# Kernel optimization log

Hardware: AMD Instinct MI355X
Metric: run time of the kernel (lower is better)

## Reference

```python
import jax, jax.numpy as jnp
import numpy as np

B, S, I = 32, 256, 256      # batch, seq_len, input_size
H, N, C, O = 512, 128, 64, 256  # lstm hidden, mem addresses, content bits, output
P = 4 * C + 12              # head params: read(k,beta,g,s3,gamma) + write(same + erase + add)
EPS = 1e-8


def setup_inputs() -> dict:
    key = jax.random.key(0)
    ks = jax.random.split(key, 8)
    sc = 0.05
    return {
        "inputs_BxSxI": jax.random.normal(ks[0], (B, S, I), jnp.float32),
        "W_ih": jax.random.normal(ks[1], (4 * H, I + C), jnp.float32) * sc,
        "W_hh": jax.random.normal(ks[2], (4 * H, H), jnp.float32) * sc,
        "b_lstm": jnp.zeros((4 * H,), jnp.float32),
        "W_head": jax.random.normal(ks[3], (P, H), jnp.float32) * sc,
        "b_head": jnp.zeros((P,), jnp.float32),
        "W_out": jax.random.normal(ks[4], (O, H + C), jnp.float32) * sc,
        "b_out": jnp.zeros((O,), jnp.float32),
    }


def _address(k, beta, g, s, gamma, w_prev, M):
    """NTM addressing: content (cosine sim * beta softmax) -> gate -> circular shift -> sharpen."""
    Mn = M / (jnp.linalg.norm(M, axis=-1, keepdims=True) + EPS)   # [B,N,C]
    kn = k / (jnp.linalg.norm(k, axis=-1, keepdims=True) + EPS)   # [B,C]
    wc = jax.nn.softmax(beta * jnp.einsum('bnc,bc->bn', Mn, kn), axis=-1)
    wg = g * wc + (1.0 - g) * w_prev                              # interpolation gate
    ws = (s[:, 0:1] * jnp.roll(wg, -1, axis=-1)                   # 3-tap circular conv shift
          + s[:, 1:2] * wg
          + s[:, 2:3] * jnp.roll(wg, 1, axis=-1))
    wp = (ws + EPS) ** gamma                                      # sharpening, gamma >= 1
    return wp / jnp.sum(wp, axis=-1, keepdims=True)


def _forward(x, W_ih, W_hh, b_lstm, W_head, b_head, W_out, b_out):
    Bv = x.shape[0]
    splits = np.cumsum([C, 1, 1, 3, 1, C, 1, 1, 3, 1, C]).tolist()

    def step(state, x_t):
        M, w_r, w_w, r, h, c = state
        # LSTM controller on [input, prev_read]
        gates = jnp.concatenate([x_t, r], -1) @ W_ih.T + h @ W_hh.T + b_lstm
        gi, gf, gg, go = jnp.split(gates, 4, axis=-1)
        c = jax.nn.sigmoid(gf) * c + jax.nn.sigmoid(gi) * jnp.tanh(gg)
        h = jax.nn.sigmoid(go) * jnp.tanh(c)
        # interface parameters
        p = h @ W_head.T + b_head
        (k_r, b_r, g_r, s_r, gm_r,
         k_w, b_w, g_w, s_w, gm_w, e_w, a_w) = jnp.split(p, splits, axis=-1)
        w_r = _address(k_r, jax.nn.softplus(b_r), jax.nn.sigmoid(g_r),
                       jax.nn.softmax(s_r, axis=-1), 1.0 + jax.nn.softplus(gm_r), w_r, M)
        w_w = _address(k_w, jax.nn.softplus(b_w), jax.nn.sigmoid(g_w),
                       jax.nn.softmax(s_w, axis=-1), 1.0 + jax.nn.softplus(gm_w), w_w, M)
        # write (erase then add), then read
        e = jax.nn.sigmoid(e_w)
        M = M * (1.0 - w_w[:, :, None] * e[:, None, :]) + w_w[:, :, None] * a_w[:, None, :]
        r = jnp.einsum('bn,bnc->bc', w_r, M)
        out = jnp.concatenate([h, r], -1) @ W_out.T + b_out
        return (M, w_r, w_w, r, h, c), out

    w0 = jnp.zeros((Bv, N), jnp.float32).at[:, 0].set(1.0)
    init = (jnp.full((Bv, N, C), 0.01, jnp.float32), w0, w0,
            jnp.zeros((Bv, C), jnp.float32),
            jnp.zeros((Bv, H), jnp.float32), jnp.zeros((Bv, H), jnp.float32))
    _, outs = jax.lax.scan(step, init, jnp.swapaxes(x, 0, 1))  # [S,B,O]
    return jnp.swapaxes(outs, 0, 1)                            # [B,S,O]


def reference(inputs_BxSxI, W_ih, W_hh, b_lstm, W_head, b_head, W_out, b_out):
    return _forward(inputs_BxSxI, W_ih, W_hh, b_lstm, W_head, b_head, W_out, b_out)
```

## Files before the change

### kernel.cpp

```cpp
#include <hip/hip_runtime.h>
#include <hip/hip_fp16.h>
#include <math.h>

#define B_  32
#define S_  256
#define I_  256
#define H_  512
#define N_  128
#define C_  64
#define O_  256
#define P_  268
#define K_  832
#define HB  (H_*B_)
#define EPSX 1e-8f
#define NBLK 160
#define NPB  32
#define NGATE 128

#define OFF_XT   0
#define SZ_XT    (S_*I_*B_)
#define OFF_HA   (OFF_XT + SZ_XT)
#define SZ_HA    ((S_+1)*H_*B_)
#define OFF_RA   (OFF_HA + SZ_HA)
#define SZ_RA    ((S_+1)*C_*B_)
#define OFF_CT   (OFF_RA + SZ_RA)
#define SZ_CT    (H_*B_)
#define OFF_M    (OFF_CT + SZ_CT)
#define SZ_M     (B_*N_*C_)
#define OFF_WR   (OFF_M + SZ_M)
#define SZ_W     (B_*N_)
#define OFF_WW   (OFF_WR + SZ_W)
#define OFF_BAR  (OFF_WW + SZ_W)
#define SZ_BAR   8192
#define OFF_WOT  (OFF_BAR + SZ_BAR)
#define SZ_WOT   ((H_+C_)*O_)
#define OFF_WHH  (OFF_WOT + SZ_WOT)
#define SZ_WHH   ((P_*H_)/2)

__device__ __forceinline__ float sigm(float x) { return 1.f / (1.f + expf(-x)); }
__device__ __forceinline__ float splus(float x) {
    return fmaxf(x, 0.f) + log1pf(expf(-fabsf(x)));
}
__device__ __forceinline__ float wave_max(float v) {
    #pragma unroll
    for (int s = 1; s < 64; s <<= 1) v = fmaxf(v, __shfl_xor(v, s, 64));
    return v;
}
__device__ __forceinline__ float wave_sum(float v) {
    #pragma unroll
    for (int s = 1; s < 64; s <<= 1) v += __shfl_xor(v, s, 64);
    return v;
}

__device__ __forceinline__ void junk16(float& s) {
    #pragma unroll
    for (int d = 0; d < 16; ++d) s = fmaf(s, 1.0000001f, 1e-9f);
    asm volatile("" : "+v"(s));
}

__device__ __forceinline__ void wait_flags(unsigned* flags, int nf, unsigned tgt,
                                           volatile unsigned* ldsp, int tid)
{
    const int wv = tid >> 6, ln = tid & 63;
    if (wv < 2) {
        int idx = wv * 64 + ln;
        if (idx >= nf) idx = nf - 1;
        unsigned* p = &flags[idx * 16];
        float s = 1.f;
        for (;;) {
            unsigned v = __hip_atomic_load(p, __ATOMIC_RELAXED,
                                           __HIP_MEMORY_SCOPE_AGENT);
            if (__all((int)(v >= tgt))) break;
            junk16(s);
        }
        if (ln == 0) ldsp[wv] = tgt;
    } else {
        float s = (float)(tid + 1);
        while (ldsp[0] < tgt || ldsp[1] < tgt) junk16(s);
    }
    __syncthreads();
}

__global__ __launch_bounds__(256)
void prep_kernel(const float* __restrict__ x, const float* __restrict__ Wout,
                 const float* __restrict__ Whead, float* __restrict__ ws)
{
    int g = blockIdx.x * 256 + threadIdx.x;
    if (g < SZ_XT) {
        int b = g & 31, k = (g >> 5) & 255, t = g >> 13;
        ws[OFF_XT + g] = x[b * (S_*I_) + t * I_ + k];
        return;
    }
    g -= SZ_XT;
    if (g < SZ_WOT) {
        int o = g & 255, k = g >> 8;
        ws[OFF_WOT + g] = Wout[o * (H_ + C_) + k];
        return;
    }
    g -= SZ_WOT;
    if (g < HB)      { ws[OFF_HA + g] = 0.f;   return; }
    g -= HB;
    if (g < C_*B_)   { ws[OFF_RA + g] = 0.f;   return; }
    g -= C_*B_;
    if (g < SZ_CT)   { ws[OFF_CT + g] = 0.f;   return; }
    g -= SZ_CT;
    if (g < SZ_M)    { ws[OFF_M  + g] = 0.01f; return; }
    g -= SZ_M;
    if (g < 2*SZ_W)  { ws[OFF_WR + g] = 0.f;   return; }
    g -= 2*SZ_W;
    if (g < SZ_BAR)  { ws[OFF_BAR + g] = 0.f;  return; }
    g -= SZ_BAR;
    if (g < P_ * H_) {
        ((__half*)(ws + OFF_WHH))[g] = __float2half(Whead[g]);
        return;
    }
}

#define GEMM_STEP(khat, ap) {                                             \
    const float4 a0 = *(const float4*)(ap);                               \
    const float4 a1 = *(const float4*)((ap) + 4);                         \
    const float2 w01 = *(const float2*)&Wt[(khat) * 18 + (rg << 2)];      \
    const float2 w23 = *(const float2*)&Wt[(khat) * 18 + (rg << 2) + 2];  \
    const float wv[4] = {w01.x, w01.y, w23.x, w23.y};                     \
    const float av[8] = {a0.x, a0.y, a0.z, a0.w, a1.x, a1.y, a1.z, a1.w}; \
    _Pragma("unroll")                                                     \
    for (int j = 0; j < 4; ++j)                                           \
        _Pragma("unroll")                                                 \
        for (int bb = 0; bb < 8; ++bb)                                    \
            acc[j][bb] += wv[j] * av[bb]; }

__global__ __launch_bounds__(512)
void ntm_loop(const float* __restrict__ Wih, const float* __restrict__ Whh,
              const float* __restrict__ bl,  const float* __restrict__ bhead,
              float* __restrict__ ws)
{
    float* xT  = ws + OFF_XT;
    float* hA  = ws + OFF_HA;
    float* rA  = ws + OFF_RA;
    float* Mem = ws + OFF_M;
    unsigned* bar = (unsigned*)(ws + OFF_BAR);
    unsigned* flag_h = bar;
    unsigned* flag_r = bar + 4096;
    const unsigned short* whH = (const unsigned short*)(ws + OFF_WHH);

    __shared__ float Wt[K_ * 18];
    __shared__ float p_lds[P_];
    __shared__ float wldsR[128];
    __shared__ float wldsW[128];
    __shared__ float h_lds[H_];
    __shared__ unsigned syncf[4];

    const int tid  = threadIdx.x;
    const int bi   = blockIdx.x;
    const bool isPB = (bi < NPB);
    const int gi   = bi - NPB;

    if (tid < 4) syncf[tid] = 0;

    if (!isPB) {
        for (int idx = tid; idx < K_ * 16; idx += 512) {
            int rl = idx & 15, k = idx >> 4;
            int row = (rl & 3) * H_ + gi * 4 + (rl >> 2);
            float v = (k < I_ + C_) ? Wih[row * (I_ + C_) + k]
                                    : Whh[row * H_ + (k - (I_ + C_))];
            Wt[k * 18 + rl] = v;
        }
    } else if (tid < N_) {
        wldsR[tid] = (tid == 0) ? 1.f : 0.f;
        wldsW[tid] = (tid == 0) ? 1.f : 0.f;
    }
    __syncthreads();

    const int pair = tid >> 5;
    const int ks   = tid & 31;
    const int rg   = pair >> 2;
    const int bg   = pair & 3;
    const int b0   = bg * 8;

    float acc[4][8];
    float cr[8] = {0,0,0,0,0,0,0,0};
    float bI = 0, bF = 0, bG = 0, bO = 0;
    if (!isPB && ks == 0) {
        const int unit = gi * 4 + rg;
        bI = bl[unit];        bF = bl[H_ + unit];
        bG = bl[2*H_ + unit]; bO = bl[3*H_ + unit];
    }

    if (!isPB) {
        #pragma unroll
        for (int j = 0; j < 4; ++j)
            #pragma unroll
            for (int bb = 0; bb < 8; ++bb) acc[j][bb] = 0.f;
        const float* xs = xT;
        const float* hs = hA;
        #pragma unroll
        for (int i = 0; i < 8; ++i) {
            const int k = ks + (i << 5);
            GEMM_STEP(k, xs + k * B_ + b0);
        }
        #pragma unroll
        for (int i = 0; i < 16; ++i) {
            const int k = ks + (i << 5);
            GEMM_STEP(320 + k, hs + k * B_ + b0);
        }

        for (int t = 0; t < S_; ++t) {
            wait_flags(flag_r, NPB, (unsigned)t, &syncf[0], tid);

            const float* rs = rA + (size_t)t * C_ * B_;
            #pragma unroll
            for (int i = 0; i < 2; ++i) {
                const int k = ks + (i << 5);
                GEMM_STEP(256 + k, rs + k * B_ + b0);
            }
            #pragma unroll
            for (int j = 0; j < 4; ++j)
                #pragma unroll
                for (int bb = 0; bb < 8; ++bb) {
                    float v = acc[j][bb];
                    v += __shfl_xor(v, 16, 64);
                    v += __shfl_xor(v, 8, 64);
                    v += __shfl_xor(v, 4, 64);
                    v += __shfl_xor(v, 2, 64);
                    v += __shfl_xor(v, 1, 64);
                    acc[j][bb] = v;
                }
            if (ks == 0) {
                const int unit = gi * 4 + rg;
                #pragma unroll
                for (int bb = 0; bb < 8; ++bb) {
                    const int b = b0 + bb;
                    float gI = acc[0][bb] + bI;
                    float gF = acc[1][bb] + bF;
                    float gG = acc[2][bb] + bG;
                    float gO = acc[3][bb] + bO;
                    float cN = sigm(gF) * cr[bb] + sigm(gI) * tanhf(gG);
                    float hN = sigm(gO) * tanhf(cN);
                    cr[bb] = cN;
                    __hip_atomic_store(&hA[(size_t)(t + 1) * HB + unit * B_ + b],
                                       hN, __ATOMIC_RELAXED,
                                       __HIP_MEMORY_SCOPE_AGENT);
                }
            }
            __syncthreads();
            if (tid == 0) {
                asm volatile("s_waitcnt vmcnt(0) lgkmcnt(0)" ::: "memory");
                __hip_atomic_store(&flag_h[gi * 16], (unsigned)(t + 1),
                                   __ATOMIC_RELAXED, __HIP_MEMORY_SCOPE_AGENT);
            }
            wait_flags(flag_h, NGATE, (unsigned)(t + 1), &syncf[2], tid);

            #pragma unroll
            for (int j = 0; j < 4; ++j)
                #pragma unroll
                for (int bb = 0; bb < 8; ++bb) acc[j][bb] = 0.f;
            if (t + 1 < S_) {
                const float* xs2 = xT + (size_t)(t + 1) * I_ * B_;
                const float* hs2 = hA + (size_t)(t + 1) * HB;
                #pragma unroll
                for (int i = 0; i < 8; ++i) {
                    const int k = ks + (i << 5);
                    GEMM_STEP(k, xs2 + k * B_ + b0);
                }
                #pragma unroll
                for (int i = 0; i < 16; ++i) {
                    const int k = ks + (i << 5);
                    GEMM_STEP(320 + k, hs2 + k * B_ + b0);
                }
            }
        }
        return;
    }

    const int b = bi;
    float* Mb = Mem + (size_t)b * N_ * C_;
    for (int t = 0; t < S_; ++t) {
        wait_flags(flag_h, NGATE, (unsigned)(t + 1), &syncf[0], tid);

        const float* hs = hA + (size_t)(t + 1) * HB;
        h_lds[tid] = __hip_atomic_load(&hs[tid * B_ + b], __ATOMIC_RELAXED,
                                       __HIP_MEMORY_SCOPE_AGENT);
        __syncthreads();

        {
            const int sub  = tid & 1;
            const int row0 = tid >> 1;
            const float* hb = &h_lds[sub * 256];
            #pragma unroll
            for (int rep = 0; rep < 2; ++rep) {
                const int row = (rep == 0) ? row0
                              : ((row0 < P_ - 256) ? row0 + 256 : -1);
                if (row >= 0) {
                    const unsigned short* wrow = whH + row * H_ + sub * 256;
                    float acch = 0.f;
                    #pragma unroll 4
                    for (int k2 = 0; k2 < 256; k2 += 8) {
                        float4 raw = *(const float4*)&wrow[k2];
                        const __half2* hp = (const __half2*)&raw;
                        float2 f0 = __half22float2(hp[0]);
                        float2 f1 = __half22float2(hp[1]);
                        float2 f2 = __half22float2(hp[2]);
                        float2 f3 = __half22float2(hp[3]);
                        acch += f0.x * hb[k2]     + f0.y * hb[k2 + 1]
                              + f1.x * hb[k2 + 2] + f1.y * hb[k2 + 3]
                              + f2.x * hb[k2 + 4] + f2.y * hb[k2 + 5]
                              + f3.x * hb[k2 + 6] + f3.y * hb[k2 + 7];
                    }
                    acch += __shfl_xor(acch, 1, 64);
                    if (sub == 0) p_lds[row] = acch + bhead[row];
                }
            }
        }
        __syncthreads();

        {
            float* wtmpA = h_lds;
            float* sbufA = h_lds + 256;
            const int grp = (tid >> 7) & 1;
            const int l   = tid & 127;
            const bool act256 = (tid < 256);
            const int o = grp ? 70 : 0;
            const int widx = (tid >> 6) & 1;

            float z = 0.f, gate = 0.f, s0 = 0.f, s1 = 0.f, s2 = 0.f,
                  gamma = 1.f;
            if (act256) {
                float beta = splus(p_lds[o + 64]);
                gate = sigm(p_lds[o + 65]);
                float sa = p_lds[o + 66], sbv = p_lds[o + 67],
                      sc = p_lds[o + 68];
                float sm3 = fmaxf(sa, fmaxf(sbv, sc));
                float ea = __expf(sa - sm3), eb = __expf(sbv - sm3),
                      ec = __expf(sc - sm3);
                float es3 = ea + eb + ec;
                s0 = ea / es3; s1 = eb / es3; s2 = ec / es3;
                gamma = 1.f + splus(p_lds[o + 69]);
                float kk = 0.f;
                #pragma unroll 8
                for (int c = 0; c < C_; ++c) {
                    float kv = p_lds[o + c]; kk += kv * kv;
                }
                const float knorm = sqrtf(kk) + EPSX;
                float dot = 0.f, mm = 0.f;
                #pragma unroll
                for (int c = 0; c < C_; c += 4) {
                    float4 m4 = *(const float4*)&Mb[l * C_ + c];
                    dot += m4.x * p_lds[o + c]     + m4.y * p_lds[o + c + 1]
                         + m4.z * p_lds[o + c + 2] + m4.w * p_lds[o + c + 3];
                    mm  += m4.x * m4.x + m4.y * m4.y + m4.z * m4.z
                         + m4.w * m4.w;
                }
                z = beta * (dot / ((sqrtf(mm) + EPSX) * knorm));
            }
            float zm = wave_max(z);
            if (act256 && (tid & 63) == 0) sbufA[grp * 8 + widx] = zm;
            __syncthreads();
            const float zmax = fmaxf(sbufA[grp * 8], sbufA[grp * 8 + 1]);
            float ev = act256 ? __expf(z - zmax) : 0.f;
            float es = wave_sum(ev);
            if (act256 && (tid & 63) == 0) sbufA[grp * 8 + 2 + widx] = es;
            __syncthreads();
            const float esum = sbufA[grp * 8 + 2] + sbufA[grp * 8 + 3];
            if (act256) {
                float wc = ev / esum;
                float wprev = grp ? wldsW[l] : wldsR[l];
                wtmpA[grp * 128 + l] = gate * wc + (1.f - gate) * wprev;
            }
            __syncthreads();
            float wp = 0.f;
            if (act256) {
                float wsft = s0 * wtmpA[grp * 128 + ((l + 1) & 127)]
                           + s1 * wtmpA[grp * 128 + l]
                           + s2 * wtmpA[grp * 128 + ((l - 1) & 127)];
                wp = __powf(wsft + EPSX, gamma);
            }
            float ps = wave_sum(wp);
            if (act256 && (tid & 63) == 0) sbufA[grp * 8 + 4 + widx] = ps;
            __syncthreads();
            const float psum = sbufA[grp * 8 + 4] + sbufA[grp * 8 + 5];
            if (act256) {
                float wn = wp / psum;
                if (grp) wldsW[l] = wn; else wldsR[l] = wn;
            }
            __syncthreads();
        }

        for (int idx = tid; idx < (N_ * C_) / 4; idx += 512) {
            const int n = idx >> 4;
            const int c = (idx & 15) << 2;
            const float wwn = wldsW[n];
            float4 m4 = *(float4*)&Mb[n * C_ + c];
            m4.x = m4.x * (1.f - wwn * sigm(p_lds[140 + c]))     + wwn * p_lds[204 + c];
            m4.y = m4.y * (1.f - wwn * sigm(p_lds[140 + c + 1])) + wwn * p_lds[204 + c + 1];
            m4.z = m4.z * (1.f - wwn * sigm(p_lds[140 + c + 2])) + wwn * p_lds[204 + c + 2];
            m4.w = m4.w * (1.f - wwn * sigm(p_lds[140 + c + 3])) + wwn * p_lds[204 + c + 3];
            *(float4*)&Mb[n * C_ + c] = m4;
        }
        __syncthreads();

        {
            const int c = tid >> 3, ns = tid & 7;
            float accr = 0.f;
            #pragma unroll
            for (int i = 0; i < 16; ++i) {
                const int n = ns + 8 * i;
                accr += wldsR[n] * Mb[n * C_ + c];
            }
            accr += __shfl_xor(accr, 4, 64);
            accr += __shfl_xor(accr, 2, 64);
            accr += __shfl_xor(accr, 1, 64);
            if (ns == 0)
                __hip_atomic_store(&rA[(size_t)(t + 1) * C_ * B_ + c * B_ + b],
                                   accr, __ATOMIC_RELAXED,
                                   __HIP_MEMORY_SCOPE_AGENT);
        }
        __syncthreads();
        if (tid == 0) {
            asm volatile("s_waitcnt vmcnt(0) lgkmcnt(0)" ::: "memory");
            __hip_atomic_store(&flag_r[b * 16], (unsigned)(t + 1),
                               __ATOMIC_RELAXED, __HIP_MEMORY_SCOPE_AGENT);
        }
    }
}

__global__ __launch_bounds__(256)
void out_kernel(const float* __restrict__ ws, const float* __restrict__ bout,
                float* __restrict__ out)
{
    __shared__ float actL[(H_ + C_) * 16];
    const float* hA  = ws + OFF_HA;
    const float* rA  = ws + OFF_RA;
    const float* WoT = ws + OFF_WOT;
    const int t   = blockIdx.x >> 1;
    const int bh  = blockIdx.x & 1;
    const int tid = threadIdx.x;

    for (int idx = tid; idx < (H_ + C_) * 16; idx += 256) {
        const int k = idx >> 4, bl2 = idx & 15, b = bh * 16 + bl2;
        float v = (k < H_) ? hA[(size_t)(t + 1) * HB + k * B_ + b]
                           : rA[(size_t)(t + 1) * C_ * B_ + (k - H_) * B_ + b];
        actL[k * 16 + bl2] = v;
    }
    __syncthreads();

    const int ot = tid & 63, bt = tid >> 6;
    const int o0 = ot * 4, bl0 = bt * 4;
    float acc[4][4] = {{0,0,0,0},{0,0,0,0},{0,0,0,0},{0,0,0,0}};
    for (int k = 0; k < H_ + C_; ++k) {
        const float4 w4 = *(const float4*)&WoT[k * O_ + o0];
        const float4 a4 = *(const float4*)&actL[k * 16 + bl0];
        const float wv[4] = {w4.x, w4.y, w4.z, w4.w};
        const float av[4] = {a4.x, a4.y, a4.z, a4.w};
        #pragma unroll
        for (int j = 0; j < 4; ++j)
            #pragma unroll
            for (int bb = 0; bb < 4; ++bb)
                acc[j][bb] += wv[j] * av[bb];
    }
    const float4 bo = *(const float4*)&bout[o0];
    #pragma unroll
    for (int bb = 0; bb < 4; ++bb) {
        const int b = bh * 16 + bl0 + bb;
        float4 res;
        res.x = acc[0][bb] + bo.x;
        res.y = acc[1][bb] + bo.y;
        res.z = acc[2][bb] + bo.z;
        res.w = acc[3][bb] + bo.w;
        *(float4*)&out[((size_t)b * S_ + t) * O_ + o0] = res;
    }
}

extern "C" void kernel_launch(void* const* d_in, const int* in_sizes, int n_in,
                              void* d_out, int out_size, void* d_ws, size_t ws_size,
                              hipStream_t stream)
{
    const float* x    = (const float*)d_in[0];
    const float* Wih  = (const float*)d_in[1];
    const float* Whh  = (const float*)d_in[2];
    const float* bl   = (const float*)d_in[3];
    const float* Whd  = (const float*)d_in[4];
    const float* bhd  = (const float*)d_in[5];
    const float* Wout = (const float*)d_in[6];
    const float* bout = (const float*)d_in[7];
    float* ws  = (float*)d_ws;
    float* out = (float*)d_out;

    prep_kernel<<<10529, 256, 0, stream>>>(x, Wout, Whd, ws);

    void* args[] = { (void*)&Wih, (void*)&Whh, (void*)&bl,
                     (void*)&bhd, (void*)&ws };
    (void)hipLaunchCooperativeKernel((void*)ntm_loop, dim3(NBLK), dim3(512), args, 0, stream);

    out_kernel<<<512, 256, 0, stream>>>(ws, bout, out);
}
```

Before: 7.115 ms.

## Keep NTM memory in LDS, fuse read into write, pack h stores

The memory matrix for each batch now lives in shared memory, reusing the weight-tile buffer with padded stride 68, instead of global workspace. The read vector is accumulated with LDS atomics inside the erase/add loop, which removes a separate read pass. The gate blocks write h as 64-bit packed atomic stores, and the spin-wait filler now uses four independent FMA chains. This cuts global memory traffic on the serial per-step critical path, at the cost of LDS atomic contention and changed floating-point summation order.

```diff
diff --git a/kernel.cpp b/kernel.cpp
--- a/kernel.cpp
+++ b/kernel.cpp
@@ -16,6 +16,7 @@
 #define NBLK 160
 #define NPB  32
 #define NGATE 128
+#define MST  68
 
 #define OFF_XT   0
 #define SZ_XT    (S_*I_*B_)
@@ -52,31 +53,35 @@
     return v;
 }
 
-__device__ __forceinline__ void junk16(float& s) {
+__device__ __forceinline__ void junkf(float& s0, float& s1, float& s2, float& s3) {
     #pragma unroll
-    for (int d = 0; d < 16; ++d) s = fmaf(s, 1.0000001f, 1e-9f);
-    asm volatile("" : "+v"(s));
+    for (int d = 0; d < 4; ++d) {
+        s0 = fmaf(s0, 1.0000001f, 1e-9f);
+        s1 = fmaf(s1, 1.0000002f, 2e-9f);
+        s2 = fmaf(s2, 1.0000003f, 3e-9f);
+        s3 = fmaf(s3, 1.0000004f, 4e-9f);
+    }
+    asm volatile("" : "+v"(s0), "+v"(s1), "+v"(s2), "+v"(s3));
 }
 
 __device__ __forceinline__ void wait_flags(unsigned* flags, int nf, unsigned tgt,
                                            volatile unsigned* ldsp, int tid)
 {
     const int wv = tid >> 6, ln = tid & 63;
+    float s0 = 1.f, s1 = 2.f, s2 = 3.f, s3 = (float)(tid + 1);
     if (wv < 2) {
         int idx = wv * 64 + ln;
         if (idx >= nf) idx = nf - 1;
         unsigned* p = &flags[idx * 16];
-        float s = 1.f;
         for (;;) {
             unsigned v = __hip_atomic_load(p, __ATOMIC_RELAXED,
                                            __HIP_MEMORY_SCOPE_AGENT);
             if (__all((int)(v >= tgt))) break;
-            junk16(s);
+            junkf(s0, s1, s2, s3);
         }
         if (ln == 0) ldsp[wv] = tgt;
     } else {
-        float s = (float)(tid + 1);
-        while (ldsp[0] < tgt || ldsp[1] < tgt) junk16(s);
+        while (ldsp[0] < tgt || ldsp[1] < tgt) junkf(s0, s1, s2, s3);
     }
     __syncthreads();
 }
@@ -137,7 +142,6 @@
     float* xT  = ws + OFF_XT;
     float* hA  = ws + OFF_HA;
     float* rA  = ws + OFF_RA;
-    float* Mem = ws + OFF_M;
     unsigned* bar = (unsigned*)(ws + OFF_BAR);
     unsigned* flag_h = bar;
     unsigned* flag_r = bar + 4096;
@@ -148,6 +152,7 @@
     __shared__ float wldsR[128];
     __shared__ float wldsW[128];
     __shared__ float h_lds[H_];
+    __shared__ float r_acc[C_];
     __shared__ unsigned syncf[4];
 
     const int tid  = threadIdx.x;
@@ -156,6 +161,8 @@
     const int gi   = bi - NPB;
 
     if (tid < 4) syncf[tid] = 0;
+
+    float* Mlds = Wt;
 
     if (!isPB) {
         for (int idx = tid; idx < K_ * 16; idx += 512) {
@@ -165,9 +172,17 @@
                                     : Whh[row * H_ + (k - (I_ + C_))];
             Wt[k * 18 + rl] = v;
         }
-    } else if (tid < N_) {
-        wldsR[tid] = (tid == 0) ? 1.f : 0.f;
-        wldsW[tid] = (tid == 0) ? 1.f : 0.f;
+    } else {
+        if (tid < N_) {
+            wldsR[tid] = (tid == 0) ? 1.f : 0.f;
+            wldsW[tid] = (tid == 0) ? 1.f : 0.f;
+        }
+        for (int idx = tid; idx < (N_ * C_) / 4; idx += 512) {
+            const int n = idx >> 4;
+            const int c = (idx & 15) << 2;
+            float4 m4 = {0.01f, 0.01f, 0.01f, 0.01f};
+            *(float4*)&Mlds[n * MST + c] = m4;
+        }
     }
     __syncthreads();
 
@@ -227,19 +242,24 @@
                 }
             if (ks == 0) {
                 const int unit = gi * 4 + rg;
+                float hv[8];
                 #pragma unroll
                 for (int bb = 0; bb < 8; ++bb) {
-                    const int b = b0 + bb;
                     float gI = acc[0][bb] + bI;
                     float gF = acc[1][bb] + bF;
                     float gG = acc[2][bb] + bG;
                     float gO = acc[3][bb] + bO;
                     float cN = sigm(gF) * cr[bb] + sigm(gI) * tanhf(gG);
-                    float hN = sigm(gO) * tanhf(cN);
+                    hv[bb] = sigm(gO) * tanhf(cN);
                     cr[bb] = cN;
-                    __hip_atomic_store(&hA[(size_t)(t + 1) * HB + unit * B_ + b],
-                                       hN, __ATOMIC_RELAXED,
-                                       __HIP_MEMORY_SCOPE_AGENT);
+                }
+                float* dst = &hA[(size_t)(t + 1) * HB + unit * B_ + b0];
+                #pragma unroll
+                for (int q = 0; q < 4; ++q) {
+                    union { float f[2]; unsigned long long u; } pk;
+                    pk.f[0] = hv[2 * q]; pk.f[1] = hv[2 * q + 1];
+                    __hip_atomic_store((unsigned long long*)(dst + 2 * q), pk.u,
+                                       __ATOMIC_RELAXED, __HIP_MEMORY_SCOPE_AGENT);
                 }
             }
             __syncthreads();
@@ -273,13 +293,13 @@
     }
 
     const int b = bi;
-    float* Mb = Mem + (size_t)b * N_ * C_;
     for (int t = 0; t < S_; ++t) {
         wait_flags(flag_h, NGATE, (unsigned)(t + 1), &syncf[0], tid);
 
         const float* hs = hA + (size_t)(t + 1) * HB;
         h_lds[tid] = __hip_atomic_load(&hs[tid * B_ + b], __ATOMIC_RELAXED,
                                        __HIP_MEMORY_SCOPE_AGENT);
+        if (tid < C_) r_acc[tid] = 0.f;
         __syncthreads();
 
         {
@@ -344,7 +364,7 @@
                 float dot = 0.f, mm = 0.f;
                 #pragma unroll
                 for (int c = 0; c < C_; c += 4) {
-                    float4 m4 = *(const float4*)&Mb[l * C_ + c];
+                    float4 m4 = *(const float4*)&Mlds[l * MST + c];
                     dot += m4.x * p_lds[o + c]     + m4.y * p_lds[o + c + 1]
                          + m4.z * p_lds[o + c + 2] + m4.w * p_lds[o + c + 3];
                     mm  += m4.x * m4.x + m4.y * m4.y + m4.z * m4.z
@@ -389,31 +409,24 @@
             const int n = idx >> 4;
             const int c = (idx & 15) << 2;
             const float wwn = wldsW[n];
-            float4 m4 = *(float4*)&Mb[n * C_ + c];
+            const float wrn = wldsR[n];
+            float4 m4 = *(float4*)&Mlds[n * MST + c];
             m4.x = m4.x * (1.f - wwn * sigm(p_lds[140 + c]))     + wwn * p_lds[204 + c];
             m4.y = m4.y * (1.f - wwn * sigm(p_lds[140 + c + 1])) + wwn * p_lds[204 + c + 1];
             m4.z = m4.z * (1.f - wwn * sigm(p_lds[140 + c + 2])) + wwn * p_lds[204 + c + 2];
             m4.w = m4.w * (1.f - wwn * sigm(p_lds[140 + c + 3])) + wwn * p_lds[204 + c + 3];
-            *(float4*)&Mb[n * C_ + c] = m4;
+            *(float4*)&Mlds[n * MST + c] = m4;
+            atomicAdd(&r_acc[c],     wrn * m4.x);
+            atomicAdd(&r_acc[c + 1], wrn * m4.y);
+            atomicAdd(&r_acc[c + 2], wrn * m4.z);
+            atomicAdd(&r_acc[c + 3], wrn * m4.w);
         }
         __syncthreads();
 
-        {
-            const int c = tid >> 3, ns = tid & 7;
-            float accr = 0.f;
-            #pragma unroll
-            for (int i = 0; i < 16; ++i) {
-                const int n = ns + 8 * i;
-                accr += wldsR[n] * Mb[n * C_ + c];
-            }
-            accr += __shfl_xor(accr, 4, 64);
-            accr += __shfl_xor(accr, 2, 64);
-            accr += __shfl_xor(accr, 1, 64);
-            if (ns == 0)
-                __hip_atomic_store(&rA[(size_t)(t + 1) * C_ * B_ + c * B_ + b],
-                                   accr, __ATOMIC_RELAXED,
-                                   __HIP_MEMORY_SCOPE_AGENT);
-        }
+        if (tid < C_)
+            __hip_atomic_store(&rA[(size_t)(t + 1) * C_ * B_ + tid * B_ + b],
+                               r_acc[tid], __ATOMIC_RELAXED,
+                               __HIP_MEMORY_SCOPE_AGENT);
         __syncthreads();
         if (tid == 0) {
             asm volatile("s_waitcnt vmcnt(0) lgkmcnt(0)" ::: "memory");
```

Result: slower. 9.029 ms (+26.9%).
